# Optimization experiments

Measured on AMD Instinct MI355X. Metric: run time of the kernel, lower is better.

## Reference

```python
import jax, jax.numpy as jnp
import numpy as np

N_ATOMS, N_BONDS, B = 3072, 12288, 64
D, H, L = 256, 8, 4
AF, BF = 74, 12
HD = D // H
EPS = 1e-5


def layer_norm(x, g, b):
    m = jnp.mean(x, -1, keepdims=True)
    v = jnp.mean((x - m) ** 2, -1, keepdims=True)
    return (x - m) / jnp.sqrt(v + EPS) * g + b


def mha(x, in_w, in_b, out_w, out_b, mask=None):
    # torch nn.MultiheadAttention with packed in_proj, batch of 1 sequence
    n = x.shape[0]
    qkv = x @ in_w.T + in_b                      # [n, 3D]
    q, k, v = jnp.split(qkv, 3, axis=-1)
    q = q.reshape(n, H, HD)
    k = k.reshape(n, H, HD)
    v = v.reshape(n, H, HD)
    scores = jnp.einsum('qhd,khd->hqk', q, k) / jnp.asarray(np.sqrt(HD), x.dtype)
    if mask is not None:
        scores = jnp.where(mask[None], scores, jnp.asarray(-1e9, x.dtype))
    att = jax.nn.softmax(scores, axis=-1)
    out = jnp.einsum('hqk,khd->qhd', att, v).reshape(n, D)
    return out @ out_w.T + out_b


def setup_inputs() -> dict:
    key = jax.random.key(0)
    ks = jax.random.split(key, 12)
    s = 0.05
    return {
        'atom_features': jax.random.normal(ks[0], (N_ATOMS, AF), jnp.float32),
        'bond_features': jax.random.normal(ks[1], (N_BONDS, BF), jnp.float32),
        'edge_indices': jax.random.randint(ks[2], (2, N_BONDS), 0, N_ATOMS),
        'batch_idx': jnp.sort(jax.random.randint(ks[3], (N_ATOMS,), 0, B)),
        'atom_w': jax.random.normal(ks[4], (D, AF), jnp.float32) * s,
        'atom_b': jnp.zeros((D,), jnp.float32),
        'bond_w': jax.random.normal(ks[5], (D, BF), jnp.float32) * s,
        'bond_b': jnp.zeros((D,), jnp.float32),
        'conv_w': jax.random.normal(ks[6], (L, D, 2 * D), jnp.float32) * s,
        'conv_b': jnp.zeros((L, D), jnp.float32),
        'attn_in_w': jax.random.normal(ks[7], (L, 3 * D, D), jnp.float32) * s,
        'attn_in_b': jnp.zeros((L, 3 * D), jnp.float32),
        'attn_out_w': jax.random.normal(ks[8], (L, D, D), jnp.float32) * s,
        'attn_out_b': jnp.zeros((L, D), jnp.float32),
        'ln_g': jnp.ones((L, D), jnp.float32),
        'ln_b': jnp.zeros((L, D), jnp.float32),
        'gattn_in_w': jax.random.normal(ks[9], (3 * D, D), jnp.float32) * s,
        'gattn_in_b': jnp.zeros((3 * D,), jnp.float32),
        'gattn_out_w': jax.random.normal(ks[10], (D, D), jnp.float32) * s,
        'gattn_out_b': jnp.zeros((D,), jnp.float32),
        'gn_g': jnp.ones((D,), jnp.float32),
        'gn_b': jnp.zeros((D,), jnp.float32),
    }


def reference(atom_features, bond_features, edge_indices, batch_idx,
              atom_w, atom_b, bond_w, bond_b, conv_w, conv_b,
              attn_in_w, attn_in_b, attn_out_w, attn_out_b, ln_g, ln_b,
              gattn_in_w, gattn_in_b, gattn_out_w, gattn_out_b, gn_g, gn_b):
    atom_h = atom_features @ atom_w.T + atom_b       # [N, D]
    bond_h = bond_features @ bond_w.T + bond_b       # [E, D]
    src, tgt = edge_indices[0], edge_indices[1]
    for i in range(L):
        # gather -> concat -> linear -> relu -> scatter-add
        messages = jnp.concatenate([atom_h[src] + bond_h, atom_h[tgt]], axis=-1)
        messages = jax.nn.relu(messages @ conv_w[i].T + conv_b[i])
        aggregated = jnp.zeros_like(atom_h).at[tgt].add(messages)
        # self-attention over all atoms as a single sequence (as in source)
        attended = mha(atom_h, attn_in_w[i], attn_in_b[i], attn_out_w[i], attn_out_b[i])
        atom_h = layer_norm(atom_h + aggregated + attended, ln_g[i], ln_b[i])
    # per-graph pooled attention == full attention masked to same-graph pairs
    same_graph = batch_idx[:, None] == batch_idx[None, :]
    pooled = mha(atom_h, gattn_in_w, gattn_in_b, gattn_out_w, gattn_out_b, mask=same_graph)
    pooled = layer_norm(pooled, gn_g, gn_b)
    sums = jax.ops.segment_sum(pooled, batch_idx, num_segments=B)
    counts = jax.ops.segment_sum(jnp.ones((pooled.shape[0],), pooled.dtype), batch_idx, num_segments=B)
    return sums / jnp.maximum(counts, 1.0)[:, None]   # empty graphs -> zeros, as in source
```

## Files before the change

### kernel.cpp

```cpp
#include <hip/hip_runtime.h>
#include <hip/hip_bf16.h>
#include <math.h>

#define NATOMS 3072
#define NBONDS 12288
#define NGRAPH 64
#define DIM 256
#define NH 8
#define HDIM 32
#define NLAYER 4
#define AFD 74
#define BFD 12
#define LNEPS 1e-5f
#define HSZ (NATOMS * HDIM)

typedef __attribute__((ext_vector_type(8))) short bf16x8;
typedef __attribute__((ext_vector_type(4))) short s16x4;
typedef __attribute__((ext_vector_type(4))) float f32x4;

static __device__ __forceinline__ short f2bf(float x) {
  union { float f; unsigned u; } v; v.f = x;
  unsigned r = v.u + 0x7fff + ((v.u >> 16) & 1);
  return (short)(r >> 16);
}

static __device__ __forceinline__ size_t afrag(int m, int c) {
  return ((size_t)(m >> 4) * 8 + (c >> 5)) * 512 + (m & 15) * 32 + (c & 31);
}

static __device__ __forceinline__ void gemm_core(
    const short* __restrict__ arow, const short* __restrict__ wch, f32x4* acc) {
  bf16x8 Xall[8];
  #pragma unroll
  for (int kc = 0; kc < 8; ++kc) Xall[kc] = *(const bf16x8*)(arow + kc * 512);
  bf16x8 Wb[2][4];
  #pragma unroll
  for (int sub = 0; sub < 4; ++sub) Wb[0][sub] = *(const bf16x8*)(wch + sub * 512);
  #pragma unroll
  for (int kc = 0; kc < 8; ++kc) {
    const int cur = kc & 1, nxt = cur ^ 1;
    if (kc < 7) {
      #pragma unroll
      for (int sub = 0; sub < 4; ++sub)
        Wb[nxt][sub] = *(const bf16x8*)(wch + (kc + 1) * 2048 + sub * 512);
    }
    __builtin_amdgcn_sched_barrier(0);
    #pragma unroll
    for (int sub = 0; sub < 4; ++sub)
      acc[sub] = __builtin_amdgcn_mfma_f32_16x16x32_bf16(Wb[cur][sub], Xall[kc], acc[sub], 0, 0, 0);
  }
}

#define CONVW_N8 65536
#define INW_N8   98304
#define OUTW_N8  32768
#define GINW_N8  24576
#define GOUTW_N8 8192
#define REPK_TOT (CONVW_N8 + INW_N8 + OUTW_N8 + GINW_N8 + GOUTW_N8)

static __device__ __forceinline__ void repack_one(
    const float* __restrict__ W, short* __restrict__ out, int kcShift, int o8) {
  const int g = o8 & 3, lq = (o8 >> 2) & 15, sub = (o8 >> 6) & 3;
  const int chunk = o8 >> 8;
  const int kc = chunk & ((1 << kcShift) - 1);
  const int nt = chunk >> kcShift;
  const int K = 32 << kcShift;
  const int n = nt * 64 + sub * 16 + lq;
  const int c = kc * 32 + g * 8;
  const float* src = W + (size_t)n * K + c;
  bf16x8 o;
  #pragma unroll
  for (int j = 0; j < 8; ++j) o[j] = f2bf(src[j]);
  ((bf16x8*)out)[o8] = o;
}

__global__ __launch_bounds__(256) void repack_all_kernel(
    const float* __restrict__ conv_w, const float* __restrict__ in_w,
    const float* __restrict__ out_w, const float* __restrict__ gin_w,
    const float* __restrict__ gout_w, short* __restrict__ conv_wb,
    short* __restrict__ in_wb, short* __restrict__ out_wb,
    short* __restrict__ gin_wb, short* __restrict__ gout_wb) {
  int o8 = blockIdx.x * 256 + threadIdx.x;
  if (o8 >= REPK_TOT) return;
  if (o8 < CONVW_N8) { repack_one(conv_w, conv_wb, 4, o8); return; }
  o8 -= CONVW_N8;
  if (o8 < INW_N8) { repack_one(in_w, in_wb, 3, o8); return; }
  o8 -= INW_N8;
  if (o8 < OUTW_N8) { repack_one(out_w, out_wb, 3, o8); return; }
  o8 -= OUTW_N8;
  if (o8 < GINW_N8) { repack_one(gin_w, gin_wb, 3, o8); return; }
  o8 -= GINW_N8;
  repack_one(gout_w, gout_wb, 3, o8);
}

__global__ __launch_bounds__(256) void proj_hist_kernel(
    const float* __restrict__ afeat, const float* __restrict__ aw,
    const float* __restrict__ ab, float* __restrict__ atom_h,
    short* __restrict__ atom_hb, const float* __restrict__ bfeat,
    const float* __restrict__ bw, const float* __restrict__ bb,
    short* __restrict__ bond_hb, const int* __restrict__ tgt,
    int* __restrict__ counts) {
  const int idx = blockIdx.x, t = threadIdx.x;
  if (idx < NATOMS) {
    __shared__ float x[AFD];
    if (t < AFD) x[t] = afeat[idx * AFD + t];
    __syncthreads();
    float acc = ab[t];
    const float* wr = aw + t * AFD;
    for (int k = 0; k < AFD; ++k) acc = fmaf(wr[k], x[k], acc);
    atom_h[idx * DIM + t] = acc;
    atom_hb[afrag(idx, t)] = f2bf(acc);
  } else if (idx < NATOMS + NBONDS) {
    const int e = idx - NATOMS;
    __shared__ float xb[BFD];
    if (t < BFD) xb[t] = bfeat[e * BFD + t];
    __syncthreads();
    float acc = bb[t];
    const float* wr = bw + t * BFD;
    #pragma unroll
    for (int k = 0; k < BFD; ++k) acc = fmaf(wr[k], xb[k], acc);
    bond_hb[afrag(e, t)] = f2bf(acc);
  } else {
    const int e = (idx - NATOMS - NBONDS) * 256 + t;
    if (e < NBONDS) atomicAdd(&counts[tgt[e]], 1);
  }
}

__global__ __launch_bounds__(256) void scan_kernel(
    const int* __restrict__ counts, int* __restrict__ rowptr,
    int* __restrict__ cursor) {
  __shared__ int part[256];
  const int t = threadIdx.x;
  int loc[12], s = 0;
  #pragma unroll
  for (int j = 0; j < 12; ++j) { loc[j] = counts[t * 12 + j]; s += loc[j]; }
  part[t] = s;
  __syncthreads();
  for (int o = 1; o < 256; o <<= 1) {
    const int v = (t >= o) ? part[t - o] : 0;
    __syncthreads();
    part[t] += v;
    __syncthreads();
  }
  int running = part[t] - s;
  #pragma unroll
  for (int j = 0; j < 12; ++j) {
    rowptr[t * 12 + j] = running;
    cursor[t * 12 + j] = running;
    running += loc[j];
  }
  if (t == 255) rowptr[NATOMS] = running;
}

__global__ __launch_bounds__(256) void scatter_kernel(
    const int* __restrict__ tgt, int* __restrict__ cursor,
    int* __restrict__ elist) {
  const int e = blockIdx.x * 256 + threadIdx.x;
  if (e < NBONDS) {
    const int pos = atomicAdd(&cursor[tgt[e]], 1);
    elist[pos] = e;
  }
}

__global__ __launch_bounds__(256) void layer_front_kernel(
    const short* __restrict__ atom_hb, const short* __restrict__ bond_hb,
    const short* __restrict__ cw, const short* __restrict__ inw,
    const float* __restrict__ inb, float* __restrict__ B1,
    float* __restrict__ G1, float* __restrict__ G2,
    short* __restrict__ Qb, short* __restrict__ Kff, short* __restrict__ Vtf,
    float qscale) {
  const int t = threadIdx.x;
  const int w = t >> 6, l = t & 63;
  const int lq = l & 15, g = l >> 4;
  const int lof = lq * 32 + g * 8;
  const int idx = blockIdx.x;
  f32x4 acc[4] = {{0.f,0.f,0.f,0.f},{0.f,0.f,0.f,0.f},{0.f,0.f,0.f,0.f},{0.f,0.f,0.f,0.f}};

  if (idx < 768) {
    const int by = idx / 384, bx = idx % 384;
    const int mrow = bx * 32 + (w & 1) * 16 + lq;
    const int nbase = by * 128 + (w >> 1) * 64;
    gemm_core(bond_hb + (size_t)(mrow >> 4) * 8 * 512 + lof,
              cw + (size_t)(nbase >> 6) * 16 * 2048 + lof, acc);
    #pragma unroll
    for (int sub = 0; sub < 4; ++sub) {
      const int n = nbase + sub * 16 + g * 4;
      *(float4*)&B1[(size_t)mrow * DIM + n] =
          make_float4(acc[sub][0], acc[sub][1], acc[sub][2], acc[sub][3]);
    }
  } else if (idx < 1152) {
    const int i2 = idx - 768;
    const int bx = i2 % 96, by = i2 / 96;
    const int mrow = bx * 32 + (w & 1) * 16 + lq;
    const int nbase = by * 128 + (w >> 1) * 64;
    const int half = nbase >> 8, nl = nbase & 255;
    gemm_core(atom_hb + (size_t)(mrow >> 4) * 8 * 512 + lof,
              cw + ((size_t)(nl >> 6) * 16 + half * 8) * 2048 + lof, acc);
    float* C = half ? G2 : G1;
    #pragma unroll
    for (int sub = 0; sub < 4; ++sub) {
      const int n = nl + sub * 16 + g * 4;
      *(float4*)&C[(size_t)mrow * DIM + n] =
          make_float4(acc[sub][0], acc[sub][1], acc[sub][2], acc[sub][3]);
    }
  } else {
    const int i3 = idx - 1152;
    const int bx = i3 % 96, by = i3 / 96;
    const int mrow = bx * 32 + (w & 1) * 16 + lq;
    const int nbase = by * 128 + (w >> 1) * 64;
    gemm_core(atom_hb + (size_t)(mrow >> 4) * 8 * 512 + lof,
              inw + (size_t)(nbase >> 6) * 8 * 2048 + lof, acc);
    const int key = mrow;
    #pragma unroll
    for (int sub = 0; sub < 4; ++sub) {
      const int n = nbase + sub * 16 + g * 4;
      const float4 b4 = *(const float4*)&inb[n];
      float4 v = make_float4(acc[sub][0] + b4.x, acc[sub][1] + b4.y,
                             acc[sub][2] + b4.z, acc[sub][3] + b4.w);
      if (n < 256) {
        s16x4 o;
        o[0] = f2bf(v.x * qscale); o[1] = f2bf(v.y * qscale);
        o[2] = f2bf(v.z * qscale); o[3] = f2bf(v.w * qscale);
        *(s16x4*)&Qb[afrag(mrow, n)] = o;
      } else if (n < 512) {
        const int d = n - 256, h = d >> 5, dd = d & 31;
        const size_t base = (size_t)h * HSZ + (size_t)(key >> 6) * 2048 +
                            (size_t)((key & 63) >> 4) * 512 +
                            ((dd >> 3) * 16 + (key & 15)) * 8 + (dd & 7);
        s16x4 o;
        o[0] = f2bf(v.x); o[1] = f2bf(v.y); o[2] = f2bf(v.z); o[3] = f2bf(v.w);
        *(s16x4*)&Kff[base] = o;
      } else {
        const int d = n - 512, h = d >> 5;
        const int kt = (key & 63) >> 5, gg = (key & 31) >> 3, j = key & 7;
        const int hh = (d & 31) >> 4;
        const size_t base = (size_t)h * HSZ + (size_t)(key >> 6) * 2048 +
                            (size_t)(kt * 2 + hh) * 512 + gg * 128 + j;
        Vtf[base + (size_t)((d + 0) & 15) * 8] = f2bf(v.x);
        Vtf[base + (size_t)((d + 1) & 15) * 8] = f2bf(v.y);
        Vtf[base + (size_t)((d + 2) & 15) * 8] = f2bf(v.z);
        Vtf[base + (size_t)((d + 3) & 15) * 8] = f2bf(v.w);
      }
    }
  }
}

template <bool MASKED>
static __device__ __forceinline__ void attn_body(
    int qtile, int h, const short* __restrict__ Qb,
    const short* __restrict__ Kff, const short* __restrict__ Vtf,
    const int* __restrict__ bidx, short* __restrict__ outbf) {
  __shared__ short Ps[4][2][16 * 72];
  __shared__ float Comb[3][64][18];

  const int t = threadIdx.x;
  const int wid = t >> 6;
  const int l = t & 63;
  const int lq = l & 15;
  const int g = l >> 4;
  const int qt0 = qtile * 32;

  const bf16x8 Qf0 = *(const bf16x8*)(Qb + ((size_t)(qt0 >> 4) * 8 + h) * 512 + lq * 32 + g * 8);
  const bf16x8 Qf1 = *(const bf16x8*)(Qb + ((size_t)(qt0 >> 4) * 8 + 8 + h) * 512 + lq * 32 + g * 8);
  const int qg0 = MASKED ? bidx[qt0 + lq] : 0;
  const int qg1 = MASKED ? bidx[qt0 + 16 + lq] : 0;

  bf16x8 OnesF;
  #pragma unroll
  for (int j = 0; j < 8; ++j) OnesF[j] = (short)0x3F80;

  const short* kh = Kff + (size_t)h * HSZ + l * 8;
  const short* vh = Vtf + (size_t)h * HSZ + l * 8;

  f32x4 accO[2][2] = {{{0.f,0.f,0.f,0.f},{0.f,0.f,0.f,0.f}},
                      {{0.f,0.f,0.f,0.f},{0.f,0.f,0.f,0.f}}};
  f32x4 accL[2] = {{0.f,0.f,0.f,0.f},{0.f,0.f,0.f,0.f}};

  const int kbeg = wid * (NATOMS / 4);
  const int kend = kbeg + NATOMS / 4;

  bf16x8 Kf[2][4];
  bf16x8 Vf[2][4];
  int4 KBv[2][4];

#define LOAD_TILE(buf, kc)                                                      \
  {                                                                             \
    const size_t tb = (size_t)((kc) >> 6) * 2048;                               \
    _Pragma("unroll")                                                           \
    for (int kk = 0; kk < 4; ++kk)                                              \
      Kf[buf][kk] = *(const bf16x8*)(kh + tb + kk * 512);                       \
    _Pragma("unroll")                                                           \
    for (int ff = 0; ff < 4; ++ff)                                              \
      Vf[buf][ff] = *(const bf16x8*)(vh + tb + ff * 512);                       \
    if (MASKED) {                                                               \
      _Pragma("unroll")                                                         \
      for (int kk = 0; kk < 4; ++kk)                                            \
        KBv[buf][kk] = *(const int4*)(bidx + (kc) + kk * 16 + g * 4);           \
    }                                                                           \
  }

  LOAD_TILE(0, kbeg);

  for (int k0 = kbeg; k0 < kend; k0 += 128) {
    #pragma unroll
    for (int ph = 0; ph < 2; ++ph) {
      const int kcur = k0 + ph * 64;
      int kn = kcur + 64;
      if (kn >= kend) kn = kbeg;
      const int pb = ph ^ 1;
      LOAD_TILE(pb, kn);
      __builtin_amdgcn_sched_barrier(0);

      #pragma unroll
      for (int qt = 0; qt < 2; ++qt) {
        const bf16x8 Qf = qt ? Qf1 : Qf0;
        const int qg = qt ? qg1 : qg0;
        short* myPs = Ps[wid][qt];
        f32x4 s[4];
        #pragma unroll
        for (int kk = 0; kk < 4; ++kk)
          s[kk] = __builtin_amdgcn_mfma_f32_16x16x32_bf16(
              Kf[ph][kk], Qf, (f32x4){0.f, 0.f, 0.f, 0.f}, 0, 0, 0);
        #pragma unroll
        for (int kk = 0; kk < 4; ++kk) {
          float p0 = __builtin_amdgcn_exp2f(s[kk][0]);
          float p1 = __builtin_amdgcn_exp2f(s[kk][1]);
          float p2 = __builtin_amdgcn_exp2f(s[kk][2]);
          float p3 = __builtin_amdgcn_exp2f(s[kk][3]);
          if (MASKED) {
            const int4 kb = KBv[ph][kk];
            p0 = (kb.x == qg) ? p0 : 0.f;
            p1 = (kb.y == qg) ? p1 : 0.f;
            p2 = (kb.z == qg) ? p2 : 0.f;
            p3 = (kb.w == qg) ? p3 : 0.f;
          }
          unsigned u0, u1;
          asm("v_cvt_pk_bf16_f32 %0, %1, %2" : "=v"(u0) : "v"(p0), "v"(p1));
          asm("v_cvt_pk_bf16_f32 %0, %1, %2" : "=v"(u1) : "v"(p2), "v"(p3));
          *(uint2*)&myPs[lq * 72 + kk * 16 + g * 4] = make_uint2(u0, u1);
        }
      }

      #pragma unroll
      for (int qt = 0; qt < 2; ++qt) {
        #pragma unroll
        for (int kt = 0; kt < 2; ++kt) {
          const bf16x8 Pf = *(const bf16x8*)&Ps[wid][qt][lq * 72 + kt * 32 + g * 8];
          #pragma unroll
          for (int hh = 0; hh < 2; ++hh)
            accO[qt][hh] = __builtin_amdgcn_mfma_f32_16x16x32_bf16(
                Vf[ph][kt * 2 + hh], Pf, accO[qt][hh], 0, 0, 0);
          accL[qt] = __builtin_amdgcn_mfma_f32_16x16x32_bf16(OnesF, Pf, accL[qt], 0, 0, 0);
        }
      }
    }
  }
#undef LOAD_TILE

  if (wid > 0) {
    #pragma unroll
    for (int qt = 0; qt < 2; ++qt) {
      Comb[wid - 1][l][qt * 9] = accL[qt][0];
      #pragma unroll
      for (int hh = 0; hh < 2; ++hh)
        #pragma unroll
        for (int r = 0; r < 4; ++r)
          Comb[wid - 1][l][qt * 9 + 1 + hh * 4 + r] = accO[qt][hh][r];
    }
  }
  __syncthreads();
  if (wid == 0) {
    #pragma unroll
    for (int qt = 0; qt < 2; ++qt) {
      float tot = accL[qt][0];
      #pragma unroll
      for (int w2 = 0; w2 < 3; ++w2) {
        tot += Comb[w2][l][qt * 9];
        #pragma unroll
        for (int hh = 0; hh < 2; ++hh)
          #pragma unroll
          for (int r = 0; r < 4; ++r)
            accO[qt][hh][r] += Comb[w2][l][qt * 9 + 1 + hh * 4 + r];
      }
      const float inv = 1.f / tot;
      const int qrow = qt0 + qt * 16 + lq;
      #pragma unroll
      for (int hh = 0; hh < 2; ++hh) {
        s16x4 o;
        #pragma unroll
        for (int r = 0; r < 4; ++r) o[r] = f2bf(accO[qt][hh][r] * inv);
        *(s16x4*)&outbf[afrag(qrow, h * HDIM + hh * 16 + g * 4)] = o;
      }
    }
  }
}

static __device__ __forceinline__ void msg_body(
    int blk, const float* __restrict__ G1, const float* __restrict__ B1,
    const float* __restrict__ G2, const float* __restrict__ bias,
    const int* __restrict__ src, const int* __restrict__ rowptr,
    const int* __restrict__ elist, float* __restrict__ agg) {
  const int wv = threadIdx.x >> 6, lane = threadIdx.x & 63;
  const int t = blk * 4 + wv;
  const int c = lane * 4;
  const float4 bb = *(const float4*)&bias[c];
  const float4 g2 = *(const float4*)&G2[(size_t)t * DIM + c];
  const float gx = g2.x + bb.x, gy = g2.y + bb.y, gz = g2.z + bb.z, gw = g2.w + bb.w;
  float4 acc = make_float4(0.f, 0.f, 0.f, 0.f);
  const int beg = rowptr[t], end = rowptr[t + 1];
  for (int j = beg; j < end; ++j) {
    const int e = elist[j];
    const int s = src[e];
    const float4 g1 = *(const float4*)&G1[(size_t)s * DIM + c];
    const float4 b1 = *(const float4*)&B1[(size_t)e * DIM + c];
    acc.x += fmaxf(g1.x + b1.x + gx, 0.f);
    acc.y += fmaxf(g1.y + b1.y + gy, 0.f);
    acc.z += fmaxf(g1.z + b1.z + gz, 0.f);
    acc.w += fmaxf(g1.w + b1.w + gw, 0.f);
  }
  *(float4*)&agg[(size_t)t * DIM + c] = acc;
}

__global__ __launch_bounds__(256) void layer_mid_kernel(
    const short* __restrict__ Qb, const short* __restrict__ Kff,
    const short* __restrict__ Vtf, short* __restrict__ att_b,
    const float* __restrict__ G1, const float* __restrict__ B1,
    const float* __restrict__ G2, const float* __restrict__ bias,
    const int* __restrict__ src, const int* __restrict__ rowptr,
    const int* __restrict__ elist, float* __restrict__ agg) {
  const int idx = blockIdx.x;
  if (idx < 768) {
    attn_body<false>(idx % 96, idx / 96, Qb, Kff, Vtf, nullptr, att_b);
  } else {
    msg_body(idx - 768, G1, B1, G2, bias, src, rowptr, elist, agg);
  }
}

template <bool MASKED>
__global__ __launch_bounds__(256) void attn_mfma_kernel(
    const short* __restrict__ Qb, const short* __restrict__ Kff,
    const short* __restrict__ Vtf, const int* __restrict__ bidx,
    short* __restrict__ outbf) {
  attn_body<MASKED>(blockIdx.x, blockIdx.y, Qb, Kff, Vtf, bidx, outbf);
}

__global__ __launch_bounds__(256) void gemm_qkv_kernel(
    const short* __restrict__ A, const short* __restrict__ W,
    const float* __restrict__ bias, short* __restrict__ Qb,
    short* __restrict__ Kff, short* __restrict__ Vtf, float qscale) {
  const int t = threadIdx.x;
  const int w = t >> 6, l = t & 63;
  const int lq = l & 15, g = l >> 4;
  const int mrow = blockIdx.x * 32 + (w & 1) * 16 + lq;
  const int nbase = blockIdx.y * 128 + (w >> 1) * 64;
  const int lof = lq * 32 + g * 8;
  f32x4 acc[4] = {{0.f,0.f,0.f,0.f},{0.f,0.f,0.f,0.f},{0.f,0.f,0.f,0.f},{0.f,0.f,0.f,0.f}};
  gemm_core(A + (size_t)(mrow >> 4) * 8 * 512 + lof,
            W + (size_t)(nbase >> 6) * 8 * 2048 + lof, acc);
  const int key = mrow;
  #pragma unroll
  for (int sub = 0; sub < 4; ++sub) {
    const int n = nbase + sub * 16 + g * 4;
    const float4 b4 = *(const float4*)&bias[n];
    float4 v = make_float4(acc[sub][0] + b4.x, acc[sub][1] + b4.y,
                           acc[sub][2] + b4.z, acc[sub][3] + b4.w);
    if (n < 256) {
      s16x4 o;
      o[0] = f2bf(v.x * qscale); o[1] = f2bf(v.y * qscale);
      o[2] = f2bf(v.z * qscale); o[3] = f2bf(v.w * qscale);
      *(s16x4*)&Qb[afrag(mrow, n)] = o;
    } else if (n < 512) {
      const int d = n - 256, h = d >> 5, dd = d & 31;
      const size_t base = (size_t)h * HSZ + (size_t)(key >> 6) * 2048 +
                          (size_t)((key & 63) >> 4) * 512 +
                          ((dd >> 3) * 16 + (key & 15)) * 8 + (dd & 7);
      s16x4 o;
      o[0] = f2bf(v.x); o[1] = f2bf(v.y); o[2] = f2bf(v.z); o[3] = f2bf(v.w);
      *(s16x4*)&Kff[base] = o;
    } else {
      const int d = n - 512, h = d >> 5;
      const int kt = (key & 63) >> 5, gg = (key & 31) >> 3, j = key & 7;
      const int hh = (d & 31) >> 4;
      const size_t base = (size_t)h * HSZ + (size_t)(key >> 6) * 2048 +
                          (size_t)(kt * 2 + hh) * 512 + gg * 128 + j;
      Vtf[base + (size_t)((d + 0) & 15) * 8] = f2bf(v.x);
      Vtf[base + (size_t)((d + 1) & 15) * 8] = f2bf(v.y);
      Vtf[base + (size_t)((d + 2) & 15) * 8] = f2bf(v.z);
      Vtf[base + (size_t)((d + 3) & 15) * 8] = f2bf(v.w);
    }
  }
}

template <bool RESID>
__global__ __launch_bounds__(256) void outproj_ln_kernel(
    const short* __restrict__ A, const short* __restrict__ W,
    const float* __restrict__ bias, const float* __restrict__ r1,
    const float* __restrict__ r2, const float* __restrict__ g,
    const float* __restrict__ b, float* __restrict__ outf,
    short* __restrict__ outbf) {
  __shared__ float Red[4][2][16];
  const int t = threadIdx.x;
  const int w = t >> 6, l = t & 63;
  const int lq = l & 15, gg = l >> 4;
  const int mtile = blockIdx.x;
  const int mrow = mtile * 16 + lq;
  const int nbase = w * 64;
  const int lof = lq * 32 + gg * 8;
  f32x4 acc[4] = {{0.f,0.f,0.f,0.f},{0.f,0.f,0.f,0.f},{0.f,0.f,0.f,0.f},{0.f,0.f,0.f,0.f}};
  gemm_core(A + (size_t)mtile * 8 * 512 + lof,
            W + (size_t)(nbase >> 6) * 8 * 2048 + lof, acc);

  float y[4][4];
  float sp = 0.f, qp = 0.f;
  #pragma unroll
  for (int sub = 0; sub < 4; ++sub) {
    const int n = nbase + sub * 16 + gg * 4;
    const float4 b4 = *(const float4*)&bias[n];
    float4 v = make_float4(acc[sub][0] + b4.x, acc[sub][1] + b4.y,
                           acc[sub][2] + b4.z, acc[sub][3] + b4.w);
    if (RESID) {
      const size_t i2 = (size_t)mrow * DIM + n;
      const float4 a4 = *(const float4*)&r1[i2];
      const float4 c4 = *(const float4*)&r2[i2];
      v.x += a4.x + c4.x; v.y += a4.y + c4.y;
      v.z += a4.z + c4.z; v.w += a4.w + c4.w;
    }
    y[sub][0] = v.x; y[sub][1] = v.y; y[sub][2] = v.z; y[sub][3] = v.w;
    sp += (v.x + v.y) + (v.z + v.w);
    qp += (v.x * v.x + v.y * v.y) + (v.z * v.z + v.w * v.w);
  }
  sp += __shfl_xor(sp, 16); sp += __shfl_xor(sp, 32);
  qp += __shfl_xor(qp, 16); qp += __shfl_xor(qp, 32);
  if (l < 16) { Red[w][0][lq] = sp; Red[w][1][lq] = qp; }
  __syncthreads();
  const float s = Red[0][0][lq] + Red[1][0][lq] + Red[2][0][lq] + Red[3][0][lq];
  const float q = Red[0][1][lq] + Red[1][1][lq] + Red[2][1][lq] + Red[3][1][lq];
  const float mean = s * (1.f / 256.f);
  const float var = q * (1.f / 256.f) - mean * mean;
  const float rstd = rsqrtf(var + LNEPS);

  #pragma unroll
  for (int sub = 0; sub < 4; ++sub) {
    const int n = nbase + sub * 16 + gg * 4;
    const float4 g4 = *(const float4*)&g[n];
    const float4 b4 = *(const float4*)&b[n];
    float4 o;
    o.x = (y[sub][0] - mean) * rstd * g4.x + b4.x;
    o.y = (y[sub][1] - mean) * rstd * g4.y + b4.y;
    o.z = (y[sub][2] - mean) * rstd * g4.z + b4.z;
    o.w = (y[sub][3] - mean) * rstd * g4.w + b4.w;
    if (outf) *(float4*)&outf[(size_t)mrow * DIM + n] = o;
    if (outbf) {
      s16x4 ob;
      ob[0] = f2bf(o.x); ob[1] = f2bf(o.y); ob[2] = f2bf(o.z); ob[3] = f2bf(o.w);
      *(s16x4*)&outbf[afrag(mrow, n)] = ob;
    }
  }
}

__global__ __launch_bounds__(256) void pool_seg_kernel(
    const float* __restrict__ pooled, const int* __restrict__ bidx,
    float* __restrict__ out) {
  const int b = blockIdx.x, t = threadIdx.x;
  __shared__ int se[2];
  if (t < 2) {
    const int target = b + t;
    int lo = 0, hi = NATOMS;
    while (lo < hi) {
      const int mid = (lo + hi) >> 1;
      if (bidx[mid] < target) lo = mid + 1; else hi = mid;
    }
    se[t] = lo;
  }
  __syncthreads();
  const int beg = se[0], end = se[1];
  float acc = 0.f;
  for (int a = beg; a < end; ++a) acc += pooled[(size_t)a * DIM + t];
  out[(size_t)b * DIM + t] = acc / fmaxf((float)(end - beg), 1.f);
}

extern "C" void kernel_launch(void* const* d_in, const int* in_sizes, int n_in,
                              void* d_out, int out_size, void* d_ws, size_t ws_size,
                              hipStream_t stream) {
  const float* atom_features = (const float*)d_in[0];
  const float* bond_features = (const float*)d_in[1];
  const int* edge_indices = (const int*)d_in[2];
  const int* batch_idx = (const int*)d_in[3];
  const float* atom_w = (const float*)d_in[4];
  const float* atom_b = (const float*)d_in[5];
  const float* bond_w = (const float*)d_in[6];
  const float* bond_b = (const float*)d_in[7];
  const float* conv_w = (const float*)d_in[8];
  const float* conv_b = (const float*)d_in[9];
  const float* attn_in_w = (const float*)d_in[10];
  const float* attn_in_b = (const float*)d_in[11];
  const float* attn_out_w = (const float*)d_in[12];
  const float* attn_out_b = (const float*)d_in[13];
  const float* ln_g = (const float*)d_in[14];
  const float* ln_b = (const float*)d_in[15];
  const float* gattn_in_w = (const float*)d_in[16];
  const float* gattn_in_b = (const float*)d_in[17];
  const float* gattn_out_w = (const float*)d_in[18];
  const float* gattn_out_b = (const float*)d_in[19];
  const float* gn_g = (const float*)d_in[20];
  const float* gn_b = (const float*)d_in[21];

  const float QSCALE = 0.17677669529663687f * 1.4426950408889634f;

  char* wsb = (char*)d_ws;
  size_t off = 0;
  auto alloc_f = [&](size_t n) { float* p = (float*)(wsb + off); off += n * 4; return p; };
  auto alloc_s = [&](size_t n) { short* p = (short*)(wsb + off); off += n * 2; return p; };
  auto alloc_i = [&](size_t n) { int* p = (int*)(wsb + off); off += n * 4; return p; };

  float* atom_h = alloc_f((size_t)NATOMS * DIM);
  float* B1     = alloc_f((size_t)NBONDS * DIM);
  float* G1     = alloc_f((size_t)NATOMS * DIM);
  float* G2     = alloc_f((size_t)NATOMS * DIM);
  float* agg    = alloc_f((size_t)NATOMS * DIM);
  short* atom_hb = alloc_s((size_t)NATOMS * DIM);
  short* bond_hb = alloc_s((size_t)NBONDS * DIM);
  short* q_b     = alloc_s((size_t)NATOMS * DIM);
  short* kff_b   = alloc_s((size_t)NATOMS * DIM);
  short* vtf_b   = alloc_s((size_t)NATOMS * DIM);
  short* att_b   = alloc_s((size_t)NATOMS * DIM);
  short* conv_wb = alloc_s((size_t)NLAYER * DIM * 2 * DIM);
  short* in_wb   = alloc_s((size_t)NLAYER * 3 * DIM * DIM);
  short* out_wb  = alloc_s((size_t)NLAYER * DIM * DIM);
  short* gin_wb  = alloc_s((size_t)3 * DIM * DIM);
  short* gout_wb = alloc_s((size_t)DIM * DIM);
  int* counts = alloc_i(NATOMS);
  int* rowptr = alloc_i(NATOMS + 1);
  int* cursor = alloc_i(NATOMS);
  int* elist  = alloc_i(NBONDS);
  if (ws_size < off) return;
  float* pooled = B1;

  const int* src = edge_indices;
  const int* tgt = edge_indices + NBONDS;

  hipMemsetAsync(counts, 0, NATOMS * sizeof(int), stream);
  proj_hist_kernel<<<NATOMS + NBONDS + NBONDS / 256, 256, 0, stream>>>(
      atom_features, atom_w, atom_b, atom_h, atom_hb,
      bond_features, bond_w, bond_b, bond_hb, tgt, counts);
  scan_kernel<<<1, 256, 0, stream>>>(counts, rowptr, cursor);
  scatter_kernel<<<NBONDS / 256, 256, 0, stream>>>(tgt, cursor, elist);
  repack_all_kernel<<<(REPK_TOT + 255) / 256, 256, 0, stream>>>(
      conv_w, attn_in_w, attn_out_w, gattn_in_w, gattn_out_w,
      conv_wb, in_wb, out_wb, gin_wb, gout_wb);

  for (int i = 0; i < NLAYER; ++i) {
    layer_front_kernel<<<1728, 256, 0, stream>>>(
        atom_hb, bond_hb, conv_wb + (size_t)i * DIM * 2 * DIM,
        in_wb + (size_t)i * 3 * DIM * DIM, attn_in_b + (size_t)i * 3 * DIM,
        B1, G1, G2, q_b, kff_b, vtf_b, QSCALE);
    layer_mid_kernel<<<1536, 256, 0, stream>>>(
        q_b, kff_b, vtf_b, att_b, G1, B1, G2, conv_b + (size_t)i * DIM,
        src, rowptr, elist, agg);
    outproj_ln_kernel<true><<<NATOMS / 16, 256, 0, stream>>>(
        att_b, out_wb + (size_t)i * DIM * DIM, attn_out_b + (size_t)i * DIM,
        atom_h, agg, ln_g + (size_t)i * DIM, ln_b + (size_t)i * DIM,
        atom_h, atom_hb);
  }

  gemm_qkv_kernel<<<dim3(96, 6), 256, 0, stream>>>(
      atom_hb, gin_wb, gattn_in_b, q_b, kff_b, vtf_b, QSCALE);
  attn_mfma_kernel<true><<<dim3(96, 8), 256, 0, stream>>>(
      q_b, kff_b, vtf_b, batch_idx, att_b);
  outproj_ln_kernel<false><<<NATOMS / 16, 256, 0, stream>>>(
      att_b, gout_wb, gattn_out_b, nullptr, nullptr, gn_g, gn_b,
      pooled, nullptr);

  pool_seg_kernel<<<NGRAPH, 256, 0, stream>>>(pooled, batch_idx, (float*)d_out);
}
```

Baseline: 313.4 us.

## Store conv intermediates in bf16, restrict masked attention to graph key range, fuse scatter+repack

The conv GEMM outputs B1, G1 and G2 are now stored as bf16 and widened back to float in the message kernel, which halves their write and gather traffic at some cost in precision. The masked pooling attention binary-searches the sorted batch index to find the key tiles that belong to the query tile's graphs and loops only over those, instead of scanning all keys. The scatter and weight-repack kernels are merged into one launch to cut launch overhead. Pooled output gets its own buffer instead of aliasing B1.

```diff
diff --git a/kernel.cpp b/kernel.cpp
--- a/kernel.cpp
+++ b/kernel.cpp
@@ -24,6 +24,15 @@
   return (short)(r >> 16);
 }
 
+static __device__ __forceinline__ float4 bf4tof4(s16x4 v) {
+  union { unsigned u; float f; } x0, x1, x2, x3;
+  x0.u = (unsigned)(unsigned short)v[0] << 16;
+  x1.u = (unsigned)(unsigned short)v[1] << 16;
+  x2.u = (unsigned)(unsigned short)v[2] << 16;
+  x3.u = (unsigned)(unsigned short)v[3] << 16;
+  return make_float4(x0.f, x1.f, x2.f, x3.f);
+}
+
 static __device__ __forceinline__ size_t afrag(int m, int c) {
   return ((size_t)(m >> 4) * 8 + (c >> 5)) * 512 + (m & 15) * 32 + (c & 31);
 }
@@ -72,25 +81,6 @@
   #pragma unroll
   for (int j = 0; j < 8; ++j) o[j] = f2bf(src[j]);
   ((bf16x8*)out)[o8] = o;
-}
-
-__global__ __launch_bounds__(256) void repack_all_kernel(
-    const float* __restrict__ conv_w, const float* __restrict__ in_w,
-    const float* __restrict__ out_w, const float* __restrict__ gin_w,
-    const float* __restrict__ gout_w, short* __restrict__ conv_wb,
-    short* __restrict__ in_wb, short* __restrict__ out_wb,
-    short* __restrict__ gin_wb, short* __restrict__ gout_wb) {
-  int o8 = blockIdx.x * 256 + threadIdx.x;
-  if (o8 >= REPK_TOT) return;
-  if (o8 < CONVW_N8) { repack_one(conv_w, conv_wb, 4, o8); return; }
-  o8 -= CONVW_N8;
-  if (o8 < INW_N8) { repack_one(in_w, in_wb, 3, o8); return; }
-  o8 -= INW_N8;
-  if (o8 < OUTW_N8) { repack_one(out_w, out_wb, 3, o8); return; }
-  o8 -= OUTW_N8;
-  if (o8 < GINW_N8) { repack_one(gin_w, gin_wb, 3, o8); return; }
-  o8 -= GINW_N8;
-  repack_one(gout_w, gout_wb, 3, o8);
 }
 
 __global__ __launch_bounds__(256) void proj_hist_kernel(
@@ -152,21 +142,40 @@
   if (t == 255) rowptr[NATOMS] = running;
 }
 
-__global__ __launch_bounds__(256) void scatter_kernel(
-    const int* __restrict__ tgt, int* __restrict__ cursor,
-    int* __restrict__ elist) {
-  const int e = blockIdx.x * 256 + threadIdx.x;
-  if (e < NBONDS) {
-    const int pos = atomicAdd(&cursor[tgt[e]], 1);
-    elist[pos] = e;
-  }
+__global__ __launch_bounds__(256) void scatter_repack_kernel(
+    const int* __restrict__ tgt, int* __restrict__ cursor, int* __restrict__ elist,
+    const float* __restrict__ conv_w, const float* __restrict__ in_w,
+    const float* __restrict__ out_w, const float* __restrict__ gin_w,
+    const float* __restrict__ gout_w, short* __restrict__ conv_wb,
+    short* __restrict__ in_wb, short* __restrict__ out_wb,
+    short* __restrict__ gin_wb, short* __restrict__ gout_wb) {
+  const int idx = blockIdx.x;
+  if (idx < 48) {
+    const int e = idx * 256 + threadIdx.x;
+    if (e < NBONDS) {
+      const int pos = atomicAdd(&cursor[tgt[e]], 1);
+      elist[pos] = e;
+    }
+    return;
+  }
+  int o8 = (idx - 48) * 256 + threadIdx.x;
+  if (o8 >= REPK_TOT) return;
+  if (o8 < CONVW_N8) { repack_one(conv_w, conv_wb, 4, o8); return; }
+  o8 -= CONVW_N8;
+  if (o8 < INW_N8) { repack_one(in_w, in_wb, 3, o8); return; }
+  o8 -= INW_N8;
+  if (o8 < OUTW_N8) { repack_one(out_w, out_wb, 3, o8); return; }
+  o8 -= OUTW_N8;
+  if (o8 < GINW_N8) { repack_one(gin_w, gin_wb, 3, o8); return; }
+  o8 -= GINW_N8;
+  repack_one(gout_w, gout_wb, 3, o8);
 }
 
 __global__ __launch_bounds__(256) void layer_front_kernel(
     const short* __restrict__ atom_hb, const short* __restrict__ bond_hb,
     const short* __restrict__ cw, const short* __restrict__ inw,
-    const float* __restrict__ inb, float* __restrict__ B1,
-    float* __restrict__ G1, float* __restrict__ G2,
+    const float* __restrict__ inb, short* __restrict__ B1,
+    short* __restrict__ G1, short* __restrict__ G2,
     short* __restrict__ Qb, short* __restrict__ Kff, short* __restrict__ Vtf,
     float qscale) {
   const int t = threadIdx.x;
@@ -185,8 +194,10 @@
     #pragma unroll
     for (int sub = 0; sub < 4; ++sub) {
       const int n = nbase + sub * 16 + g * 4;
-      *(float4*)&B1[(size_t)mrow * DIM + n] =
-          make_float4(acc[sub][0], acc[sub][1], acc[sub][2], acc[sub][3]);
+      s16x4 o;
+      o[0] = f2bf(acc[sub][0]); o[1] = f2bf(acc[sub][1]);
+      o[2] = f2bf(acc[sub][2]); o[3] = f2bf(acc[sub][3]);
+      *(s16x4*)&B1[(size_t)mrow * DIM + n] = o;
     }
   } else if (idx < 1152) {
     const int i2 = idx - 768;
@@ -196,12 +207,14 @@
     const int half = nbase >> 8, nl = nbase & 255;
     gemm_core(atom_hb + (size_t)(mrow >> 4) * 8 * 512 + lof,
               cw + ((size_t)(nl >> 6) * 16 + half * 8) * 2048 + lof, acc);
-    float* C = half ? G2 : G1;
+    short* C = half ? G2 : G1;
     #pragma unroll
     for (int sub = 0; sub < 4; ++sub) {
       const int n = nl + sub * 16 + g * 4;
-      *(float4*)&C[(size_t)mrow * DIM + n] =
-          make_float4(acc[sub][0], acc[sub][1], acc[sub][2], acc[sub][3]);
+      s16x4 o;
+      o[0] = f2bf(acc[sub][0]); o[1] = f2bf(acc[sub][1]);
+      o[2] = f2bf(acc[sub][2]); o[3] = f2bf(acc[sub][3]);
+      *(s16x4*)&C[(size_t)mrow * DIM + n] = o;
     }
   } else {
     const int i3 = idx - 1152;
@@ -245,11 +258,10 @@
   }
 }
 
-template <bool MASKED>
-static __device__ __forceinline__ void attn_body(
+static __device__ __forceinline__ void attn_body_full(
     int qtile, int h, const short* __restrict__ Qb,
     const short* __restrict__ Kff, const short* __restrict__ Vtf,
-    const int* __restrict__ bidx, short* __restrict__ outbf) {
+    short* __restrict__ outbf) {
   __shared__ short Ps[4][2][16 * 72];
   __shared__ float Comb[3][64][18];
 
@@ -262,8 +274,6 @@
 
   const bf16x8 Qf0 = *(const bf16x8*)(Qb + ((size_t)(qt0 >> 4) * 8 + h) * 512 + lq * 32 + g * 8);
   const bf16x8 Qf1 = *(const bf16x8*)(Qb + ((size_t)(qt0 >> 4) * 8 + 8 + h) * 512 + lq * 32 + g * 8);
-  const int qg0 = MASKED ? bidx[qt0 + lq] : 0;
-  const int qg1 = MASKED ? bidx[qt0 + 16 + lq] : 0;
 
   bf16x8 OnesF;
   #pragma unroll
@@ -281,7 +291,6 @@
 
   bf16x8 Kf[2][4];
   bf16x8 Vf[2][4];
-  int4 KBv[2][4];
 
 #define LOAD_TILE(buf, kc)                                                      \
   {                                                                             \
@@ -292,11 +301,6 @@
     _Pragma("unroll")                                                           \
     for (int ff = 0; ff < 4; ++ff)                                              \
       Vf[buf][ff] = *(const bf16x8*)(vh + tb + ff * 512);                       \
-    if (MASKED) {                                                               \
-      _Pragma("unroll")                                                         \
-      for (int kk = 0; kk < 4; ++kk)                                            \
-        KBv[buf][kk] = *(const int4*)(bidx + (kc) + kk * 16 + g * 4);           \
-    }                                                                           \
   }
 
   LOAD_TILE(0, kbeg);
@@ -314,7 +318,6 @@
       #pragma unroll
       for (int qt = 0; qt < 2; ++qt) {
         const bf16x8 Qf = qt ? Qf1 : Qf0;
-        const int qg = qt ? qg1 : qg0;
         short* myPs = Ps[wid][qt];
         f32x4 s[4];
         #pragma unroll
@@ -323,17 +326,10 @@
               Kf[ph][kk], Qf, (f32x4){0.f, 0.f, 0.f, 0.f}, 0, 0, 0);
         #pragma unroll
         for (int kk = 0; kk < 4; ++kk) {
-          float p0 = __builtin_amdgcn_exp2f(s[kk][0]);
-          float p1 = __builtin_amdgcn_exp2f(s[kk][1]);
-          float p2 = __builtin_amdgcn_exp2f(s[kk][2]);
-          float p3 = __builtin_amdgcn_exp2f(s[kk][3]);
-          if (MASKED) {
-            const int4 kb = KBv[ph][kk];
-            p0 = (kb.x == qg) ? p0 : 0.f;
-            p1 = (kb.y == qg) ? p1 : 0.f;
-            p2 = (kb.z == qg) ? p2 : 0.f;
-            p3 = (kb.w == qg) ? p3 : 0.f;
-          }
+          const float p0 = __builtin_amdgcn_exp2f(s[kk][0]);
+          const float p1 = __builtin_amdgcn_exp2f(s[kk][1]);
+          const float p2 = __builtin_amdgcn_exp2f(s[kk][2]);
+          const float p3 = __builtin_amdgcn_exp2f(s[kk][3]);
           unsigned u0, u1;
           asm("v_cvt_pk_bf16_f32 %0, %1, %2" : "=v"(u0) : "v"(p0), "v"(p1));
           asm("v_cvt_pk_bf16_f32 %0, %1, %2" : "=v"(u1) : "v"(p2), "v"(p3));
@@ -395,24 +391,161 @@
   }
 }
 
+static __device__ __forceinline__ void attn_body_masked(
+    int qtile, int h, const short* __restrict__ Qb,
+    const short* __restrict__ Kff, const short* __restrict__ Vtf,
+    const int* __restrict__ bidx, short* __restrict__ outbf) {
+  __shared__ short Ps[4][2][16 * 72];
+  __shared__ float Comb[3][64][18];
+  __shared__ int srange[2];
+
+  const int t = threadIdx.x;
+  const int wid = t >> 6;
+  const int l = t & 63;
+  const int lq = l & 15;
+  const int g = l >> 4;
+  const int qt0 = qtile * 32;
+
+  if (t < 2) {
+    const int target = (t == 0) ? bidx[qt0] : (bidx[qt0 + 31] + 1);
+    int lo = 0, hi = NATOMS;
+    while (lo < hi) {
+      const int mid = (lo + hi) >> 1;
+      if (bidx[mid] < target) lo = mid + 1; else hi = mid;
+    }
+    srange[t] = lo;
+  }
+
+  const bf16x8 Qf0 = *(const bf16x8*)(Qb + ((size_t)(qt0 >> 4) * 8 + h) * 512 + lq * 32 + g * 8);
+  const bf16x8 Qf1 = *(const bf16x8*)(Qb + ((size_t)(qt0 >> 4) * 8 + 8 + h) * 512 + lq * 32 + g * 8);
+  const int qg0 = bidx[qt0 + lq];
+  const int qg1 = bidx[qt0 + 16 + lq];
+
+  bf16x8 OnesF;
+  #pragma unroll
+  for (int j = 0; j < 8; ++j) OnesF[j] = (short)0x3F80;
+
+  const short* kh = Kff + (size_t)h * HSZ + l * 8;
+  const short* vh = Vtf + (size_t)h * HSZ + l * 8;
+
+  f32x4 accO[2][2] = {{{0.f,0.f,0.f,0.f},{0.f,0.f,0.f,0.f}},
+                      {{0.f,0.f,0.f,0.f},{0.f,0.f,0.f,0.f}}};
+  f32x4 accL[2] = {{0.f,0.f,0.f,0.f},{0.f,0.f,0.f,0.f}};
+
+  __syncthreads();
+  const int t0 = srange[0] >> 6;
+  const int t1 = (srange[1] + 63) >> 6;
+
+  for (int tt = t0 + wid; tt < t1; tt += 4) {
+    const int kc = tt * 64;
+    const size_t tb = (size_t)tt * 2048;
+    bf16x8 Kf[4], Vf[4];
+    int4 KBv[4];
+    #pragma unroll
+    for (int kk = 0; kk < 4; ++kk) Kf[kk] = *(const bf16x8*)(kh + tb + kk * 512);
+    #pragma unroll
+    for (int ff = 0; ff < 4; ++ff) Vf[ff] = *(const bf16x8*)(vh + tb + ff * 512);
+    #pragma unroll
+    for (int kk = 0; kk < 4; ++kk) KBv[kk] = *(const int4*)(bidx + kc + kk * 16 + g * 4);
+
+    #pragma unroll
+    for (int qt = 0; qt < 2; ++qt) {
+      const bf16x8 Qf = qt ? Qf1 : Qf0;
+      const int qg = qt ? qg1 : qg0;
+      short* myPs = Ps[wid][qt];
+      f32x4 s[4];
+      #pragma unroll
+      for (int kk = 0; kk < 4; ++kk)
+        s[kk] = __builtin_amdgcn_mfma_f32_16x16x32_bf16(
+            Kf[kk], Qf, (f32x4){0.f, 0.f, 0.f, 0.f}, 0, 0, 0);
+      #pragma unroll
+      for (int kk = 0; kk < 4; ++kk) {
+        float p0 = __builtin_amdgcn_exp2f(s[kk][0]);
+        float p1 = __builtin_amdgcn_exp2f(s[kk][1]);
+        float p2 = __builtin_amdgcn_exp2f(s[kk][2]);
+        float p3 = __builtin_amdgcn_exp2f(s[kk][3]);
+        const int4 kb = KBv[kk];
+        p0 = (kb.x == qg) ? p0 : 0.f;
+        p1 = (kb.y == qg) ? p1 : 0.f;
+        p2 = (kb.z == qg) ? p2 : 0.f;
+        p3 = (kb.w == qg) ? p3 : 0.f;
+        unsigned u0, u1;
+        asm("v_cvt_pk_bf16_f32 %0, %1, %2" : "=v"(u0) : "v"(p0), "v"(p1));
+        asm("v_cvt_pk_bf16_f32 %0, %1, %2" : "=v"(u1) : "v"(p2), "v"(p3));
+        *(uint2*)&myPs[lq * 72 + kk * 16 + g * 4] = make_uint2(u0, u1);
+      }
+    }
+
+    #pragma unroll
+    for (int qt = 0; qt < 2; ++qt) {
+      #pragma unroll
+      for (int kt = 0; kt < 2; ++kt) {
+        const bf16x8 Pf = *(const bf16x8*)&Ps[wid][qt][lq * 72 + kt * 32 + g * 8];
+        #pragma unroll
+        for (int hh = 0; hh < 2; ++hh)
+          accO[qt][hh] = __builtin_amdgcn_mfma_f32_16x16x32_bf16(
+              Vf[kt * 2 + hh], Pf, accO[qt][hh], 0, 0, 0);
+        accL[qt] = __builtin_amdgcn_mfma_f32_16x16x32_bf16(OnesF, Pf, accL[qt], 0, 0, 0);
+      }
+    }
+  }
+
+  if (wid > 0) {
+    #pragma unroll
+    for (int qt = 0; qt < 2; ++qt) {
+      Comb[wid - 1][l][qt * 9] = accL[qt][0];
+      #pragma unroll
+      for (int hh = 0; hh < 2; ++hh)
+        #pragma unroll
+        for (int r = 0; r < 4; ++r)
+          Comb[wid - 1][l][qt * 9 + 1 + hh * 4 + r] = accO[qt][hh][r];
+    }
+  }
+  __syncthreads();
+  if (wid == 0) {
+    #pragma unroll
+    for (int qt = 0; qt < 2; ++qt) {
+      float tot = accL[qt][0];
+      #pragma unroll
+      for (int w2 = 0; w2 < 3; ++w2) {
+        tot += Comb[w2][l][qt * 9];
+        #pragma unroll
+        for (int hh = 0; hh < 2; ++hh)
+          #pragma unroll
+          for (int r = 0; r < 4; ++r)
+            accO[qt][hh][r] += Comb[w2][l][qt * 9 + 1 + hh * 4 + r];
+      }
+      const float inv = 1.f / tot;
+      const int qrow = qt0 + qt * 16 + lq;
+      #pragma unroll
+      for (int hh = 0; hh < 2; ++hh) {
+        s16x4 o;
+        #pragma unroll
+        for (int r = 0; r < 4; ++r) o[r] = f2bf(accO[qt][hh][r] * inv);
+        *(s16x4*)&outbf[afrag(qrow, h * HDIM + hh * 16 + g * 4)] = o;
+      }
+    }
+  }
+}
+
 static __device__ __forceinline__ void msg_body(
-    int blk, const float* __restrict__ G1, const float* __restrict__ B1,
-    const float* __restrict__ G2, const float* __restrict__ bias,
+    int blk, const short* __restrict__ G1, const short* __restrict__ B1,
+    const short* __restrict__ G2, const float* __restrict__ bias,
     const int* __restrict__ src, const int* __restrict__ rowptr,
     const int* __restrict__ elist, float* __restrict__ agg) {
   const int wv = threadIdx.x >> 6, lane = threadIdx.x & 63;
   const int t = blk * 4 + wv;
   const int c = lane * 4;
   const float4 bb = *(const float4*)&bias[c];
-  const float4 g2 = *(const float4*)&G2[(size_t)t * DIM + c];
+  const float4 g2 = bf4tof4(*(const s16x4*)&G2[(size_t)t * DIM + c]);
   const float gx = g2.x + bb.x, gy = g2.y + bb.y, gz = g2.z + bb.z, gw = g2.w + bb.w;
   float4 acc = make_float4(0.f, 0.f, 0.f, 0.f);
   const int beg = rowptr[t], end = rowptr[t + 1];
   for (int j = beg; j < end; ++j) {
     const int e = elist[j];
     const int s = src[e];
-    const float4 g1 = *(const float4*)&G1[(size_t)s * DIM + c];
-    const float4 b1 = *(const float4*)&B1[(size_t)e * DIM + c];
+    const float4 g1 = bf4tof4(*(const s16x4*)&G1[(size_t)s * DIM + c]);
+    const float4 b1 = bf4tof4(*(const s16x4*)&B1[(size_t)e * DIM + c]);
     acc.x += fmaxf(g1.x + b1.x + gx, 0.f);
     acc.y += fmaxf(g1.y + b1.y + gy, 0.f);
     acc.z += fmaxf(g1.z + b1.z + gz, 0.f);
@@ -424,24 +557,23 @@
 __global__ __launch_bounds__(256) void layer_mid_kernel(
     const short* __restrict__ Qb, const short* __restrict__ Kff,
     const short* __restrict__ Vtf, short* __restrict__ att_b,
-    const float* __restrict__ G1, const float* __restrict__ B1,
-    const float* __restrict__ G2, const float* __restrict__ bias,
+    const short* __restrict__ G1, const short* __restrict__ B1,
+    const short* __restrict__ G2, const float* __restrict__ bias,
     const int* __restrict__ src, const int* __restrict__ rowptr,
     const int* __restrict__ elist, float* __restrict__ agg) {
   const int idx = blockIdx.x;
   if (idx < 768) {
-    attn_body<false>(idx % 96, idx / 96, Qb, Kff, Vtf, nullptr, att_b);
+    attn_body_full(idx % 96, idx / 96, Qb, Kff, Vtf, att_b);
   } else {
     msg_body(idx - 768, G1, B1, G2, bias, src, rowptr, elist, agg);
   }
 }
 
-template <bool MASKED>
-__global__ __launch_bounds__(256) void attn_mfma_kernel(
+__global__ __launch_bounds__(256) void attn_masked_kernel(
     const short* __restrict__ Qb, const short* __restrict__ Kff,
     const short* __restrict__ Vtf, const int* __restrict__ bidx,
     short* __restrict__ outbf) {
-  attn_body<MASKED>(blockIdx.x, blockIdx.y, Qb, Kff, Vtf, bidx, outbf);
+  attn_body_masked(blockIdx.x, blockIdx.y, Qb, Kff, Vtf, bidx, outbf);
 }
 
 __global__ __launch_bounds__(256) void gemm_qkv_kernel(
@@ -614,10 +746,11 @@
   auto alloc_i = [&](size_t n) { int* p = (int*)(wsb + off); off += n * 4; return p; };
 
   float* atom_h = alloc_f((size_t)NATOMS * DIM);
-  float* B1     = alloc_f((size_t)NBONDS * DIM);
-  float* G1     = alloc_f((size_t)NATOMS * DIM);
-  float* G2     = alloc_f((size_t)NATOMS * DIM);
   float* agg    = alloc_f((size_t)NATOMS * DIM);
+  float* pooled = alloc_f((size_t)NATOMS * DIM);
+  short* B1     = alloc_s((size_t)NBONDS * DIM);
+  short* G1     = alloc_s((size_t)NATOMS * DIM);
+  short* G2     = alloc_s((size_t)NATOMS * DIM);
   short* atom_hb = alloc_s((size_t)NATOMS * DIM);
   short* bond_hb = alloc_s((size_t)NBONDS * DIM);
   short* q_b     = alloc_s((size_t)NATOMS * DIM);
@@ -634,7 +767,6 @@
   int* cursor = alloc_i(NATOMS);
   int* elist  = alloc_i(NBONDS);
   if (ws_size < off) return;
-  float* pooled = B1;
 
   const int* src = edge_indices;
   const int* tgt = edge_indices + NBONDS;
@@ -644,9 +776,8 @@
       atom_features, atom_w, atom_b, atom_h, atom_hb,
       bond_features, bond_w, bond_b, bond_hb, tgt, counts);
   scan_kernel<<<1, 256, 0, stream>>>(counts, rowptr, cursor);
-  scatter_kernel<<<NBONDS / 256, 256, 0, stream>>>(tgt, cursor, elist);
-  repack_all_kernel<<<(REPK_TOT + 255) / 256, 256, 0, stream>>>(
-      conv_w, attn_in_w, attn_out_w, gattn_in_w, gattn_out_w,
+  scatter_repack_kernel<<<48 + REPK_TOT / 256, 256, 0, stream>>>(
+      tgt, cursor, elist, conv_w, attn_in_w, attn_out_w, gattn_in_w, gattn_out_w,
       conv_wb, in_wb, out_wb, gin_wb, gout_wb);
 
   for (int i = 0; i < NLAYER; ++i) {
@@ -665,7 +796,7 @@
 
   gemm_qkv_kernel<<<dim3(96, 6), 256, 0, stream>>>(
       atom_hb, gin_wb, gattn_in_b, q_b, kff_b, vtf_b, QSCALE);
-  attn_mfma_kernel<true><<<dim3(96, 8), 256, 0, stream>>>(
+  attn_masked_kernel<<<dim3(96, 8), 256, 0, stream>>>(
       q_b, kff_b, vtf_b, batch_idx, att_b);
   outproj_ln_kernel<false><<<NATOMS / 16, 256, 0, stream>>>(
       att_b, gout_wb, gattn_out_b, nullptr, nullptr, gn_g, gn_b,
```

After: 297.3 us. 1.05x faster.
